# Performance work log

Measured on AMD Instinct MI355X. Metric: run time of the kernel, lower is better.

Reference implementation:

```python
import jax, jax.numpy as jnp
import numpy as np

NUM_EXPERTS = 8
HIDDEN = 1024
INTERMEDIATE = 2816
TOTAL_TOKENS = 4096  # 512 tokens per expert


def setup_inputs() -> dict:
    key = jax.random.key(0)
    k_x, k1, k2, k3 = jax.random.split(key, 4)
    hiddens = jax.random.normal(k_x, (TOTAL_TOKENS, HIDDEN), dtype=jnp.float32)
    # tokens assumed pre-sorted by expert; equal-sized groups here
    batch_sizes = jnp.full((NUM_EXPERTS,), TOTAL_TOKENS // NUM_EXPERTS, dtype=jnp.int64)
    w1_weight = jax.random.normal(k1, (NUM_EXPERTS, HIDDEN, INTERMEDIATE), dtype=jnp.float32)
    w2_weight = jax.random.normal(k2, (NUM_EXPERTS, INTERMEDIATE, HIDDEN), dtype=jnp.float32)
    w3_weight = jax.random.normal(k3, (NUM_EXPERTS, HIDDEN, INTERMEDIATE), dtype=jnp.float32)
    return {
        "hiddens": hiddens,
        "w1_weight": w1_weight,
        "w2_weight": w2_weight,
        "w3_weight": w3_weight,
        "batch_sizes": batch_sizes,
    }


def _grouped_moe(hiddens, w1, w2, w3, batch_sizes):
    """Grouped SwiGLU FFN: tokens are contiguous per expert (sizes = batch_sizes).

    Jit-safe formulation: map each token to its expert id, then run one masked
    dense GEMM trio per expert (small fixed expert count). Zero rows contribute
    exactly zero (silu(0)*0 == 0), so no final masking of the output is needed.
    """
    num_experts = w1.shape[0]
    total_tokens = hiddens.shape[0]
    bounds = jnp.cumsum(batch_sizes)  # [E] exclusive-right boundaries
    expert_ids = jnp.searchsorted(bounds, jnp.arange(total_tokens), side="right")  # [T]
    out = jnp.zeros((total_tokens, w2.shape[-1]), dtype=hiddens.dtype)
    for e in range(num_experts):
        mask = (expert_ids == e)[:, None]  # [T, 1]
        xe = jnp.where(mask, hiddens, 0)   # zero out other experts' tokens
        up = jax.nn.silu(xe @ w1[e]) * (xe @ w3[e])  # [T, F] SwiGLU
        out = out + up @ w2[e]             # [T, H]
    return out


def reference(hiddens, w1_weight, w2_weight, w3_weight, batch_sizes):
    return _grouped_moe(hiddens, w1_weight, w2_weight, w3_weight, batch_sizes)
```

## Files before the change

kernel.cpp:

```cpp
#include <hip/hip_runtime.h>
#include <hip/hip_bf16.h>

#define NE 8
#define HD 1024
#define ID 2816
#define TT 4096
#define BM 128
#define BK 32
#define BN1 64
#define BN2 64
#define MAXMT (TT / BM + NE)
#define NKS1 (HD / BK)
#define NKS2 (ID / BK)
#define ATILE 8192
#define GS 1040
#define BT (4 * GS)

typedef __attribute__((ext_vector_type(4))) float f32x4;
typedef __attribute__((ext_vector_type(8))) short s16x8;

__device__ __forceinline__ unsigned int f2bfpk(float lo, float hi) {
  float2 t; t.x = lo; t.y = hi;
  union { __hip_bfloat162 h2; unsigned int u; } cv;
  cv.h2 = __float22bfloat162_rn(t);
  return cv.u;
}

__device__ __forceinline__ void glds16(const void* g, void* l) {
  __builtin_amdgcn_global_load_lds(
      (const __attribute__((address_space(1))) void*)g,
      (__attribute__((address_space(3))) void*)l, 16, 0, 0);
}

__device__ __forceinline__ bool map_tile(const void* bsp, int mt, int& e,
                                         int& mstart, int& rowend) {
  const int* w = (const int*)bsp;
  bool is64 = (w[1] == 0) && (w[3] == 0) && (w[5] == 0) && (w[7] == 0) &&
              ((w[0] | w[2] | w[4] | w[6]) != 0);
  long long start = 0;
  int rem = mt;
  for (int i = 0; i < NE; ++i) {
    long long b = is64 ? ((const long long*)bsp)[i] : (long long)w[i];
    if (b < 0) b = 0;
    int tiles = (int)((b + BM - 1) / BM);
    if (rem < tiles) {
      long long m0 = start + (long long)rem * BM;
      long long me = start + b;
      if (m0 >= TT) return false;
      if (me > TT) me = TT;
      e = i; mstart = (int)m0; rowend = (int)me;
      return true;
    }
    rem -= tiles;
    start += b;
  }
  return false;
}

__global__ __launch_bounds__(256) void cvt_xt(const float* __restrict__ x,
                                              const void* __restrict__ bsp,
                                              unsigned short* __restrict__ xt) {
  int mt = blockIdx.x >> 5;
  int ks = blockIdx.x & 31;
  int e, mstart, rowend;
  if (!map_tile(bsp, mt, e, mstart, rowend)) return;
  int t = threadIdx.x;
  int lane = t & 63;
  int r = lane & 15, q = lane >> 4;
  unsigned short* ob = xt + ((size_t)mt * NKS1 + ks) * (ATILE / 2);
#pragma unroll
  for (int h = 0; h < 2; ++h) {
    int f = h * 4 + (t >> 6);
    int row = mstart + f * 16 + r;
    s16x8 o = (s16x8)0;
    if (row < rowend) {
      const float* src = x + (size_t)row * HD + ks * 32 + q * 8;
      f32x4 v0 = *(const f32x4*)src;
      f32x4 v1 = *(const f32x4*)(src + 4);
      unsigned int d0 = f2bfpk(v0[0], v0[1]), d1 = f2bfpk(v0[2], v0[3]);
      unsigned int d2 = f2bfpk(v1[0], v1[1]), d3 = f2bfpk(v1[2], v1[3]);
      o[0] = (short)d0; o[1] = (short)(d0 >> 16);
      o[2] = (short)d1; o[3] = (short)(d1 >> 16);
      o[4] = (short)d2; o[5] = (short)(d2 >> 16);
      o[6] = (short)d3; o[7] = (short)(d3 >> 16);
    }
    *(s16x8*)(ob + h * 2048 + t * 8) = o;
  }
}

__global__ __launch_bounds__(256, 3) void moe_gemm1(
    const unsigned short* __restrict__ xt, const float* __restrict__ w1,
    const float* __restrict__ w3, const void* __restrict__ bsp,
    __hip_bfloat16* __restrict__ up) {
  __shared__ __align__(16) char As[2][ATILE];
  __shared__ __align__(16) char B1s[2][BT];
  __shared__ __align__(16) char B3s[2][BT];

  const int NWG = (ID / BN1) * MAXMT;
  int bid = blockIdx.x;
  int logical = (bid & 7) * (NWG >> 3) + (bid >> 3);
  int mt = logical % MAXMT;
  int nt = logical / MAXMT;
  int e, mstart, rowend;
  if (!map_tile(bsp, mt, e, mstart, rowend)) return;
  const int n0 = nt * BN1;
  const int tid = threadIdx.x;
  const int lane = tid & 63;
  const int wv = tid >> 6;
  const int wr = wv >> 1, wc = wv & 1;
  const int q = lane >> 4, r16 = lane & 15;

  const int c4 = tid & 15, kb = tid >> 4;
  const int wbase = (c4 >> 2) * GS + (kb >> 2) * 256 + (c4 & 3) * 64 + (kb & 3) * 4;
  const char* agp = (const char*)xt + (size_t)mt * NKS1 * ATILE + tid * 16;
  const float* w1c = w1 + (size_t)e * HD * ID + (size_t)(2 * kb) * ID + n0 + c4 * 4;
  const float* w3c = w3 + (size_t)e * HD * ID + (size_t)(2 * kb) * ID + n0 + c4 * 4;

  f32x4 acc1[4][2], acc3[4][2];
#pragma unroll
  for (int i = 0; i < 4; ++i)
#pragma unroll
    for (int j = 0; j < 2; ++j) { acc1[i][j] = (f32x4)0.f; acc3[i][j] = (f32x4)0.f; }

  f32x4 Wa[4], Wb[4];

  auto gldsA = [&](int k, int buf) {
    const char* s = agp + (size_t)k * ATILE;
    char* d = &As[buf][0] + tid * 16;
    glds16(s, d);
    glds16(s + 4096, d + 4096);
  };
  auto loadB = [&](f32x4* W) {
    W[0] = *(const f32x4*)w1c;
    W[1] = *(const f32x4*)(w1c + ID);
    W[2] = *(const f32x4*)w3c;
    W[3] = *(const f32x4*)(w3c + ID);
    w1c += (size_t)BK * ID; w3c += (size_t)BK * ID;
  };
  auto storeB = [&](int buf, const f32x4* W) {
#pragma unroll
    for (int ci = 0; ci < 4; ++ci) {
      *(unsigned int*)(B1s[buf] + wbase + ci * 16) = f2bfpk(W[0][ci], W[1][ci]);
      *(unsigned int*)(B3s[buf] + wbase + ci * 16) = f2bfpk(W[2][ci], W[3][ci]);
    }
  };
  auto compute = [&](int ab, int bb) {
    s16x8 a[4], b1[2], b3[2];
#pragma unroll
    for (int i = 0; i < 4; ++i)
      a[i] = *(const s16x8*)(As[ab] + (wr * 4 + i) * 1024 + lane * 16);
#pragma unroll
    for (int j = 0; j < 2; ++j) {
      b1[j] = *(const s16x8*)(B1s[bb] + (wc * 2 + j) * GS + lane * 16);
      b3[j] = *(const s16x8*)(B3s[bb] + (wc * 2 + j) * GS + lane * 16);
    }
#pragma unroll
    for (int i = 0; i < 4; ++i)
#pragma unroll
      for (int j = 0; j < 2; ++j) {
        acc1[i][j] = __builtin_amdgcn_mfma_f32_16x16x32_bf16(a[i], b1[j], acc1[i][j], 0, 0, 0);
        acc3[i][j] = __builtin_amdgcn_mfma_f32_16x16x32_bf16(a[i], b3[j], acc3[i][j], 0, 0, 0);
      }
  };

#define G1PHASE(P, KC)                                                    \
  {                                                                       \
    const bool doG = (kt + (KC) + 1 < NKS1);                              \
    const bool doL = (kt + (KC) + 2 < NKS1);                              \
    if (doG) {                                                            \
      gldsA(kt + (KC) + 1, (P) ^ 1);                                      \
      __builtin_amdgcn_sched_barrier(0);                                  \
    }                                                                     \
    if (doL) {                                                            \
      loadB((P) ? Wb : Wa);                                               \
      __builtin_amdgcn_sched_barrier(0);                                  \
    }                                                                     \
    compute((P), (P));                                                    \
    if (doG) {                                                            \
      storeB((P) ^ 1, (P) ? Wa : Wb);                                     \
      if (doL)                                                            \
        asm volatile("s_waitcnt vmcnt(4) lgkmcnt(0)" ::: "memory");       \
      else                                                                \
        asm volatile("s_waitcnt vmcnt(0) lgkmcnt(0)" ::: "memory");       \
      __builtin_amdgcn_s_barrier();                                       \
    }                                                                     \
  }

  gldsA(0, 0);
  __builtin_amdgcn_sched_barrier(0);
  loadB(Wa);
  __builtin_amdgcn_sched_barrier(0);
  loadB(Wb);
  storeB(0, Wa);
  asm volatile("s_waitcnt vmcnt(4) lgkmcnt(0)" ::: "memory");
  __builtin_amdgcn_s_barrier();

  for (int kt = 0; kt < NKS1; kt += 2) {
    G1PHASE(0, 0)
    G1PHASE(1, 1)
  }
#undef G1PHASE

#pragma unroll
  for (int i = 0; i < 4; ++i)
#pragma unroll
    for (int r = 0; r < 4; ++r) {
      int gm = mstart + wr * 64 + i * 16 + q * 4 + r;
      if (gm < rowend) {
#pragma unroll
        for (int j = 0; j < 2; ++j) {
          float v1 = acc1[i][j][r], v3 = acc3[i][j][r];
          float s = v1 / (1.f + __expf(-v1));
          up[(size_t)gm * ID + n0 + wc * 32 + j * 16 + r16] = __float2bfloat16(s * v3);
        }
      }
    }
}

__global__ __launch_bounds__(256, 4) void moe_gemm2(
    const __hip_bfloat16* __restrict__ up, const float* __restrict__ w2,
    const void* __restrict__ bsp, float* __restrict__ out) {
  __shared__ __align__(16) char As[2][ATILE];
  __shared__ __align__(16) char Bs[2][BT];

  const int NWG = (HD / BN2) * MAXMT;
  int bid = blockIdx.x;
  int logical = (bid & 7) * (NWG >> 3) + (bid >> 3);
  int mt = logical % MAXMT;
  int nt = logical / MAXMT;
  int e, mstart, rowend;
  if (!map_tile(bsp, mt, e, mstart, rowend)) return;
  const int n0 = nt * BN2;
  const int tid = threadIdx.x;
  const int lane = tid & 63;
  const int wv = tid >> 6;
  const int wr = wv >> 1, wc = wv & 1;
  const int q = lane >> 4, r16 = lane & 15;

  const int c4 = tid & 15, kb = tid >> 4;
  const int wbase = (c4 >> 2) * GS + (kb >> 2) * 256 + (c4 & 3) * 64 + (kb & 3) * 4;
  const float* w2c = w2 + (size_t)e * ID * HD + (size_t)(2 * kb) * HD + n0 + c4 * 4;

  int row0 = mstart + (tid >> 6) * 16 + (tid & 15);
  int row1 = row0 + 64;
  row0 = row0 < TT ? row0 : TT - 1;
  row1 = row1 < TT ? row1 : TT - 1;
  const char* uc0 = (const char*)up + ((size_t)row0 * ID + q * 8) * 2;
  const char* uc1 = (const char*)up + ((size_t)row1 * ID + q * 8) * 2;

  f32x4 acc[4][2];
#pragma unroll
  for (int i = 0; i < 4; ++i)
#pragma unroll
    for (int j = 0; j < 2; ++j) acc[i][j] = (f32x4)0.f;

  f32x4 Wa[2], Wb[2];

  auto gldsA = [&](int buf) {
    char* d = &As[buf][0] + tid * 16;
    glds16(uc0, d);
    glds16(uc1, d + 4096);
    uc0 += BK * 2; uc1 += BK * 2;
  };
  auto loadB = [&](f32x4* W) {
    W[0] = *(const f32x4*)w2c;
    W[1] = *(const f32x4*)(w2c + HD);
    w2c += (size_t)BK * HD;
  };
  auto storeB = [&](int buf, const f32x4* W) {
#pragma unroll
    for (int ci = 0; ci < 4; ++ci)
      *(unsigned int*)(Bs[buf] + wbase + ci * 16) = f2bfpk(W[0][ci], W[1][ci]);
  };
  auto compute = [&](int ab, int bb) {
    s16x8 a[4], b[2];
#pragma unroll
    for (int i = 0; i < 4; ++i)
      a[i] = *(const s16x8*)(As[ab] + (wr * 4 + i) * 1024 + lane * 16);
#pragma unroll
    for (int j = 0; j < 2; ++j)
      b[j] = *(const s16x8*)(Bs[bb] + (wc * 2 + j) * GS + lane * 16);
#pragma unroll
    for (int i = 0; i < 4; ++i)
#pragma unroll
      for (int j = 0; j < 2; ++j)
        acc[i][j] = __builtin_amdgcn_mfma_f32_16x16x32_bf16(a[i], b[j], acc[i][j], 0, 0, 0);
  };

#define G2PHASE(P, KC)                                                    \
  {                                                                       \
    const bool doG = (kt + (KC) + 1 < NKS2);                              \
    const bool doL = (kt + (KC) + 2 < NKS2);                              \
    if (doG) {                                                            \
      gldsA((P) ^ 1);                                                     \
      __builtin_amdgcn_sched_barrier(0);                                  \
    }                                                                     \
    if (doL) {                                                            \
      loadB((P) ? Wb : Wa);                                               \
      __builtin_amdgcn_sched_barrier(0);                                  \
    }                                                                     \
    compute((P), (P));                                                    \
    if (doG) {                                                            \
      storeB((P) ^ 1, (P) ? Wa : Wb);                                     \
      if (doL)                                                            \
        asm volatile("s_waitcnt vmcnt(2) lgkmcnt(0)" ::: "memory");       \
      else                                                                \
        asm volatile("s_waitcnt vmcnt(0) lgkmcnt(0)" ::: "memory");       \
      __builtin_amdgcn_s_barrier();                                       \
    }                                                                     \
  }

  gldsA(0);
  __builtin_amdgcn_sched_barrier(0);
  loadB(Wa);
  __builtin_amdgcn_sched_barrier(0);
  loadB(Wb);
  storeB(0, Wa);
  asm volatile("s_waitcnt vmcnt(2) lgkmcnt(0)" ::: "memory");
  __builtin_amdgcn_s_barrier();

  for (int kt = 0; kt < NKS2; kt += 2) {
    G2PHASE(0, 0)
    G2PHASE(1, 1)
  }
#undef G2PHASE

#pragma unroll
  for (int i = 0; i < 4; ++i)
#pragma unroll
    for (int r = 0; r < 4; ++r) {
      int gm = mstart + wr * 64 + i * 16 + q * 4 + r;
      if (gm < rowend) {
#pragma unroll
        for (int j = 0; j < 2; ++j)
          out[(size_t)gm * HD + n0 + wc * 32 + j * 16 + r16] = acc[i][j][r];
      }
    }
}

extern "C" void kernel_launch(void* const* d_in, const int* in_sizes, int n_in,
                              void* d_out, int out_size, void* d_ws, size_t ws_size,
                              hipStream_t stream) {
  const float* x = (const float*)d_in[0];
  const float* w1 = (const float*)d_in[1];
  const float* w2 = (const float*)d_in[2];
  const float* w3 = (const float*)d_in[3];
  const void* bs = d_in[4];
  float* out = (float*)d_out;
  unsigned short* xt = (unsigned short*)d_ws;
  __hip_bfloat16* up =
      (__hip_bfloat16*)((char*)d_ws + (size_t)MAXMT * NKS1 * ATILE);

  hipMemsetAsync(d_out, 0, (size_t)out_size * sizeof(float), stream);

  cvt_xt<<<dim3(MAXMT * NKS1), dim3(256), 0, stream>>>(x, bs, xt);
  moe_gemm1<<<dim3((ID / BN1) * MAXMT), dim3(256), 0, stream>>>(xt, w1, w3, bs, up);
  moe_gemm2<<<dim3((HD / BN2) * MAXMT), dim3(256), 0, stream>>>(up, w2, bs, out);
}
```

Measured before the change: 199.7 us.

## Widen N tiles to 128 with 512-thread blocks and simplify B prefetch pipeline

Both grouped GEMMs move from 64-wide to 128-wide N tiles on 512-thread workgroups. Each of the 8 waves keeps the same 64x32 output sub-tile, and the global-to-LDS load work is spread across twice as many threads. The two-deep register prefetch of B is cut to a single prefetch with a full vmcnt(0) wait, which saves registers but exposes more load latency per step. s_setprio is wrapped around the MFMA block to favour compute waves, and the larger tile roughly halves how often A is re-read across N tiles, at the cost of fewer workgroups.

```diff
diff --git a/kernel.cpp b/kernel.cpp
--- a/kernel.cpp
+++ b/kernel.cpp
@@ -7,14 +7,14 @@
 #define TT 4096
 #define BM 128
 #define BK 32
-#define BN1 64
-#define BN2 64
+#define BN1 128
+#define BN2 128
 #define MAXMT (TT / BM + NE)
 #define NKS1 (HD / BK)
 #define NKS2 (ID / BK)
 #define ATILE 8192
 #define GS 1040
-#define BT (4 * GS)
+#define BT (8 * GS)
 
 typedef __attribute__((ext_vector_type(4))) float f32x4;
 typedef __attribute__((ext_vector_type(8))) short s16x8;
@@ -88,7 +88,7 @@
   }
 }
 
-__global__ __launch_bounds__(256, 3) void moe_gemm1(
+__global__ __launch_bounds__(512, 4) void moe_gemm1(
     const unsigned short* __restrict__ xt, const float* __restrict__ w1,
     const float* __restrict__ w3, const void* __restrict__ bsp,
     __hip_bfloat16* __restrict__ up) {
@@ -107,11 +107,12 @@
   const int tid = threadIdx.x;
   const int lane = tid & 63;
   const int wv = tid >> 6;
-  const int wr = wv >> 1, wc = wv & 1;
+  const int wr = wv >> 2, wc = wv & 3;
   const int q = lane >> 4, r16 = lane & 15;
 
-  const int c4 = tid & 15, kb = tid >> 4;
-  const int wbase = (c4 >> 2) * GS + (kb >> 2) * 256 + (c4 & 3) * 64 + (kb & 3) * 4;
+  const int c4 = tid & 31, kb = tid >> 5;
+  const int wbase = (c4 >> 2) * GS + (kb >> 2) * 256 + (kb & 3) * 4;
+  const int wcol = (c4 & 3) * 4;
   const char* agp = (const char*)xt + (size_t)mt * NKS1 * ATILE + tid * 16;
   const float* w1c = w1 + (size_t)e * HD * ID + (size_t)(2 * kb) * ID + n0 + c4 * 4;
   const float* w3c = w3 + (size_t)e * HD * ID + (size_t)(2 * kb) * ID + n0 + c4 * 4;
@@ -122,26 +123,23 @@
 #pragma unroll
     for (int j = 0; j < 2; ++j) { acc1[i][j] = (f32x4)0.f; acc3[i][j] = (f32x4)0.f; }
 
-  f32x4 Wa[4], Wb[4];
+  f32x4 W1[2], W3[2];
 
   auto gldsA = [&](int k, int buf) {
-    const char* s = agp + (size_t)k * ATILE;
-    char* d = &As[buf][0] + tid * 16;
-    glds16(s, d);
-    glds16(s + 4096, d + 4096);
-  };
-  auto loadB = [&](f32x4* W) {
-    W[0] = *(const f32x4*)w1c;
-    W[1] = *(const f32x4*)(w1c + ID);
-    W[2] = *(const f32x4*)w3c;
-    W[3] = *(const f32x4*)(w3c + ID);
+    glds16(agp + (size_t)k * ATILE, &As[buf][0] + tid * 16);
+  };
+  auto loadB = [&]() {
+    W1[0] = *(const f32x4*)w1c;
+    W1[1] = *(const f32x4*)(w1c + ID);
+    W3[0] = *(const f32x4*)w3c;
+    W3[1] = *(const f32x4*)(w3c + ID);
     w1c += (size_t)BK * ID; w3c += (size_t)BK * ID;
   };
-  auto storeB = [&](int buf, const f32x4* W) {
+  auto storeB = [&](int buf) {
 #pragma unroll
     for (int ci = 0; ci < 4; ++ci) {
-      *(unsigned int*)(B1s[buf] + wbase + ci * 16) = f2bfpk(W[0][ci], W[1][ci]);
-      *(unsigned int*)(B3s[buf] + wbase + ci * 16) = f2bfpk(W[2][ci], W[3][ci]);
+      *(unsigned int*)(B1s[buf] + wbase + (wcol + ci) * 16) = f2bfpk(W1[0][ci], W1[1][ci]);
+      *(unsigned int*)(B3s[buf] + wbase + (wcol + ci) * 16) = f2bfpk(W3[0][ci], W3[1][ci]);
     }
   };
   auto compute = [&](int ab, int bb) {
@@ -154,6 +152,7 @@
       b1[j] = *(const s16x8*)(B1s[bb] + (wc * 2 + j) * GS + lane * 16);
       b3[j] = *(const s16x8*)(B3s[bb] + (wc * 2 + j) * GS + lane * 16);
     }
+    __builtin_amdgcn_s_setprio(1);
 #pragma unroll
     for (int i = 0; i < 4; ++i)
 #pragma unroll
@@ -161,38 +160,31 @@
         acc1[i][j] = __builtin_amdgcn_mfma_f32_16x16x32_bf16(a[i], b1[j], acc1[i][j], 0, 0, 0);
         acc3[i][j] = __builtin_amdgcn_mfma_f32_16x16x32_bf16(a[i], b3[j], acc3[i][j], 0, 0, 0);
       }
+    __builtin_amdgcn_s_setprio(0);
   };
 
 #define G1PHASE(P, KC)                                                    \
   {                                                                       \
-    const bool doG = (kt + (KC) + 1 < NKS1);                              \
-    const bool doL = (kt + (KC) + 2 < NKS1);                              \
-    if (doG) {                                                            \
+    const bool nx = (kt + (KC) + 1 < NKS1);                               \
+    if (nx) {                                                             \
+      loadB();                                                            \
+      __builtin_amdgcn_sched_barrier(0);                                  \
       gldsA(kt + (KC) + 1, (P) ^ 1);                                      \
       __builtin_amdgcn_sched_barrier(0);                                  \
     }                                                                     \
-    if (doL) {                                                            \
-      loadB((P) ? Wb : Wa);                                               \
-      __builtin_amdgcn_sched_barrier(0);                                  \
-    }                                                                     \
     compute((P), (P));                                                    \
-    if (doG) {                                                            \
-      storeB((P) ^ 1, (P) ? Wa : Wb);                                     \
-      if (doL)                                                            \
-        asm volatile("s_waitcnt vmcnt(4) lgkmcnt(0)" ::: "memory");       \
-      else                                                                \
-        asm volatile("s_waitcnt vmcnt(0) lgkmcnt(0)" ::: "memory");       \
+    if (nx) {                                                             \
+      storeB((P) ^ 1);                                                    \
+      asm volatile("s_waitcnt vmcnt(0) lgkmcnt(0)" ::: "memory");         \
       __builtin_amdgcn_s_barrier();                                       \
     }                                                                     \
   }
 
+  loadB();
+  __builtin_amdgcn_sched_barrier(0);
   gldsA(0, 0);
-  __builtin_amdgcn_sched_barrier(0);
-  loadB(Wa);
-  __builtin_amdgcn_sched_barrier(0);
-  loadB(Wb);
-  storeB(0, Wa);
-  asm volatile("s_waitcnt vmcnt(4) lgkmcnt(0)" ::: "memory");
+  storeB(0);
+  asm volatile("s_waitcnt vmcnt(0) lgkmcnt(0)" ::: "memory");
   __builtin_amdgcn_s_barrier();
 
   for (int kt = 0; kt < NKS1; kt += 2) {
@@ -217,7 +209,7 @@
     }
 }
 
-__global__ __launch_bounds__(256, 4) void moe_gemm2(
+__global__ __launch_bounds__(512, 4) void moe_gemm2(
     const __hip_bfloat16* __restrict__ up, const float* __restrict__ w2,
     const void* __restrict__ bsp, float* __restrict__ out) {
   __shared__ __align__(16) char As[2][ATILE];
@@ -234,19 +226,17 @@
   const int tid = threadIdx.x;
   const int lane = tid & 63;
   const int wv = tid >> 6;
-  const int wr = wv >> 1, wc = wv & 1;
+  const int wr = wv >> 2, wc = wv & 3;
   const int q = lane >> 4, r16 = lane & 15;
 
-  const int c4 = tid & 15, kb = tid >> 4;
-  const int wbase = (c4 >> 2) * GS + (kb >> 2) * 256 + (c4 & 3) * 64 + (kb & 3) * 4;
+  const int c4 = tid & 31, kb = tid >> 5;
+  const int wbase = (c4 >> 2) * GS + (kb >> 2) * 256 + (kb & 3) * 4;
+  const int wcol = (c4 & 3) * 4;
   const float* w2c = w2 + (size_t)e * ID * HD + (size_t)(2 * kb) * HD + n0 + c4 * 4;
 
   int row0 = mstart + (tid >> 6) * 16 + (tid & 15);
-  int row1 = row0 + 64;
   row0 = row0 < TT ? row0 : TT - 1;
-  row1 = row1 < TT ? row1 : TT - 1;
-  const char* uc0 = (const char*)up + ((size_t)row0 * ID + q * 8) * 2;
-  const char* uc1 = (const char*)up + ((size_t)row1 * ID + q * 8) * 2;
+  const char* uc0 = (const char*)up + ((size_t)row0 * ID + ((tid >> 4) & 3) * 8) * 2;
 
   f32x4 acc[4][2];
 #pragma unroll
@@ -254,23 +244,21 @@
 #pragma unroll
     for (int j = 0; j < 2; ++j) acc[i][j] = (f32x4)0.f;
 
-  f32x4 Wa[2], Wb[2];
+  f32x4 W[2];
 
   auto gldsA = [&](int buf) {
-    char* d = &As[buf][0] + tid * 16;
-    glds16(uc0, d);
-    glds16(uc1, d + 4096);
-    uc0 += BK * 2; uc1 += BK * 2;
-  };
-  auto loadB = [&](f32x4* W) {
+    glds16(uc0, &As[buf][0] + tid * 16);
+    uc0 += BK * 2;
+  };
+  auto loadB = [&]() {
     W[0] = *(const f32x4*)w2c;
     W[1] = *(const f32x4*)(w2c + HD);
     w2c += (size_t)BK * HD;
   };
-  auto storeB = [&](int buf, const f32x4* W) {
+  auto storeB = [&](int buf) {
 #pragma unroll
     for (int ci = 0; ci < 4; ++ci)
-      *(unsigned int*)(Bs[buf] + wbase + ci * 16) = f2bfpk(W[0][ci], W[1][ci]);
+      *(unsigned int*)(Bs[buf] + wbase + (wcol + ci) * 16) = f2bfpk(W[0][ci], W[1][ci]);
   };
   auto compute = [&](int ab, int bb) {
     s16x8 a[4], b[2];
@@ -280,43 +268,37 @@
 #pragma unroll
     for (int j = 0; j < 2; ++j)
       b[j] = *(const s16x8*)(Bs[bb] + (wc * 2 + j) * GS + lane * 16);
+    __builtin_amdgcn_s_setprio(1);
 #pragma unroll
     for (int i = 0; i < 4; ++i)
 #pragma unroll
       for (int j = 0; j < 2; ++j)
         acc[i][j] = __builtin_amdgcn_mfma_f32_16x16x32_bf16(a[i], b[j], acc[i][j], 0, 0, 0);
+    __builtin_amdgcn_s_setprio(0);
   };
 
 #define G2PHASE(P, KC)                                                    \
   {                                                                       \
-    const bool doG = (kt + (KC) + 1 < NKS2);                              \
-    const bool doL = (kt + (KC) + 2 < NKS2);                              \
-    if (doG) {                                                            \
+    const bool nx = (kt + (KC) + 1 < NKS2);                               \
+    if (nx) {                                                             \
+      loadB();                                                            \
+      __builtin_amdgcn_sched_barrier(0);                                  \
       gldsA((P) ^ 1);                                                     \
       __builtin_amdgcn_sched_barrier(0);                                  \
     }                                                                     \
-    if (doL) {                                                            \
-      loadB((P) ? Wb : Wa);                                               \
-      __builtin_amdgcn_sched_barrier(0);                                  \
-    }                                                                     \
     compute((P), (P));                                                    \
-    if (doG) {                                                            \
-      storeB((P) ^ 1, (P) ? Wa : Wb);                                     \
-      if (doL)                                                            \
-        asm volatile("s_waitcnt vmcnt(2) lgkmcnt(0)" ::: "memory");       \
-      else                                                                \
-        asm volatile("s_waitcnt vmcnt(0) lgkmcnt(0)" ::: "memory");       \
+    if (nx) {                                                             \
+      storeB((P) ^ 1);                                                    \
+      asm volatile("s_waitcnt vmcnt(0) lgkmcnt(0)" ::: "memory");         \
       __builtin_amdgcn_s_barrier();                                       \
     }                                                                     \
   }
 
+  loadB();
+  __builtin_amdgcn_sched_barrier(0);
   gldsA(0);
-  __builtin_amdgcn_sched_barrier(0);
-  loadB(Wa);
-  __builtin_amdgcn_sched_barrier(0);
-  loadB(Wb);
-  storeB(0, Wa);
-  asm volatile("s_waitcnt vmcnt(2) lgkmcnt(0)" ::: "memory");
+  storeB(0);
+  asm volatile("s_waitcnt vmcnt(0) lgkmcnt(0)" ::: "memory");
   __builtin_amdgcn_s_barrier();
 
   for (int kt = 0; kt < NKS2; kt += 2) {
@@ -354,6 +336,6 @@
   hipMemsetAsync(d_out, 0, (size_t)out_size * sizeof(float), stream);
 
   cvt_xt<<<dim3(MAXMT * NKS1), dim3(256), 0, stream>>>(x, bs, xt);
-  moe_gemm1<<<dim3((ID / BN1) * MAXMT), dim3(256), 0, stream>>>(xt, w1, w3, bs, up);
-  moe_gemm2<<<dim3((HD / BN2) * MAXMT), dim3(256), 0, stream>>>(up, w2, bs, out);
-}
+  moe_gemm1<<<dim3((ID / BN1) * MAXMT), dim3(512), 0, stream>>>(xt, w1, w3, bs, up);
+  moe_gemm2<<<dim3((HD / BN2) * MAXMT), dim3(512), 0, stream>>>(up, w2, bs, out);
+}
```

New measurement: 250.0 us. 25.2% more time.

## Double M tile to 256 rows with 512-thread blocks and MFMA priority

Applied to the files above, without the earlier changes.

Raises the M tile from 128 to 256 rows and runs both GEMMs with 512-thread blocks (8 waves). Each block now reuses every converted fp32 weight tile across twice as many tokens. This halves the per-token weight global reads and the fp32-to-bf16 conversion work, which dominate since weights are fp32. In gemm1 the W1 and W3 loads are split between the two halves of the block; in gemm2 only half the threads load W2. MFMA sections are wrapped in s_setprio, and the waitcnt counts are adjusted. Risks are fewer blocks per expert, more LDS per block, and tile waste when expert groups do not fill 256 rows.

```diff
diff --git a/kernel.cpp b/kernel.cpp
--- a/kernel.cpp
+++ b/kernel.cpp
@@ -5,7 +5,7 @@
 #define HD 1024
 #define ID 2816
 #define TT 4096
-#define BM 128
+#define BM 256
 #define BK 32
 #define BN1 64
 #define BN2 64
@@ -13,6 +13,7 @@
 #define NKS1 (HD / BK)
 #define NKS2 (ID / BK)
 #define ATILE 8192
+#define TILE2 (2 * ATILE)
 #define GS 1040
 #define BT (4 * GS)
 
@@ -67,11 +68,12 @@
   int t = threadIdx.x;
   int lane = t & 63;
   int r = lane & 15, q = lane >> 4;
-  unsigned short* ob = xt + ((size_t)mt * NKS1 + ks) * (ATILE / 2);
-#pragma unroll
-  for (int h = 0; h < 2; ++h) {
-    int f = h * 4 + (t >> 6);
-    int row = mstart + f * 16 + r;
+  unsigned short* ob = xt + ((size_t)mt * NKS1 + ks) * (TILE2 / 2);
+#pragma unroll
+  for (int hh = 0; hh < 4; ++hh) {
+    int half = hh >> 1, fq = hh & 1;
+    int f = fq * 4 + (t >> 6);
+    int row = mstart + half * 128 + f * 16 + r;
     s16x8 o = (s16x8)0;
     if (row < rowend) {
       const float* src = x + (size_t)row * HD + ks * 32 + q * 8;
@@ -84,15 +86,15 @@
       o[4] = (short)d2; o[5] = (short)(d2 >> 16);
       o[6] = (short)d3; o[7] = (short)(d3 >> 16);
     }
-    *(s16x8*)(ob + h * 2048 + t * 8) = o;
-  }
-}
-
-__global__ __launch_bounds__(256, 3) void moe_gemm1(
+    *(s16x8*)(ob + half * 4096 + fq * 2048 + t * 8) = o;
+  }
+}
+
+__global__ __launch_bounds__(512, 2) void moe_gemm1(
     const unsigned short* __restrict__ xt, const float* __restrict__ w1,
     const float* __restrict__ w3, const void* __restrict__ bsp,
     __hip_bfloat16* __restrict__ up) {
-  __shared__ __align__(16) char As[2][ATILE];
+  __shared__ __align__(16) char As[2][TILE2];
   __shared__ __align__(16) char B1s[2][BT];
   __shared__ __align__(16) char B3s[2][BT];
 
@@ -110,11 +112,15 @@
   const int wr = wv >> 1, wc = wv & 1;
   const int q = lane >> 4, r16 = lane & 15;
 
-  const int c4 = tid & 15, kb = tid >> 4;
-  const int wbase = (c4 >> 2) * GS + (kb >> 2) * 256 + (c4 & 3) * 64 + (kb & 3) * 4;
-  const char* agp = (const char*)xt + (size_t)mt * NKS1 * ATILE + tid * 16;
-  const float* w1c = w1 + (size_t)e * HD * ID + (size_t)(2 * kb) * ID + n0 + c4 * 4;
-  const float* w3c = w3 + (size_t)e * HD * ID + (size_t)(2 * kb) * ID + n0 + c4 * 4;
+  const int t8 = tid & 255;
+  const int c4 = t8 & 15, kp = t8 >> 4;
+  const int wbase = (c4 >> 2) * GS + (kp >> 2) * 256 + (kp & 3) * 4;
+  const int wcol = (c4 & 3) * 4;
+  const char* agp = (const char*)xt + (size_t)mt * NKS1 * TILE2 + tid * 16;
+  const float* wsrc = ((tid & 256) ? w3 : w1) + (size_t)e * HD * ID +
+                      (size_t)(2 * kp) * ID + n0 + c4 * 4;
+  char* bdst0 = (tid & 256) ? B3s[0] : B1s[0];
+  char* bdst1 = (tid & 256) ? B3s[1] : B1s[1];
 
   f32x4 acc1[4][2], acc3[4][2];
 #pragma unroll
@@ -122,38 +128,37 @@
 #pragma unroll
     for (int j = 0; j < 2; ++j) { acc1[i][j] = (f32x4)0.f; acc3[i][j] = (f32x4)0.f; }
 
-  f32x4 Wa[4], Wb[4];
+  f32x4 Wa[2], Wb[2];
 
   auto gldsA = [&](int k, int buf) {
-    const char* s = agp + (size_t)k * ATILE;
+    const char* s = agp + (size_t)k * TILE2;
     char* d = &As[buf][0] + tid * 16;
     glds16(s, d);
-    glds16(s + 4096, d + 4096);
+    glds16(s + ATILE, d + ATILE);
   };
   auto loadB = [&](f32x4* W) {
-    W[0] = *(const f32x4*)w1c;
-    W[1] = *(const f32x4*)(w1c + ID);
-    W[2] = *(const f32x4*)w3c;
-    W[3] = *(const f32x4*)(w3c + ID);
-    w1c += (size_t)BK * ID; w3c += (size_t)BK * ID;
+    W[0] = *(const f32x4*)wsrc;
+    W[1] = *(const f32x4*)(wsrc + ID);
+    wsrc += (size_t)BK * ID;
   };
   auto storeB = [&](int buf, const f32x4* W) {
-#pragma unroll
-    for (int ci = 0; ci < 4; ++ci) {
-      *(unsigned int*)(B1s[buf] + wbase + ci * 16) = f2bfpk(W[0][ci], W[1][ci]);
-      *(unsigned int*)(B3s[buf] + wbase + ci * 16) = f2bfpk(W[2][ci], W[3][ci]);
-    }
+    char* b = buf ? bdst1 : bdst0;
+#pragma unroll
+    for (int ci = 0; ci < 4; ++ci)
+      *(unsigned int*)(b + wbase + (wcol + ci) * 16) = f2bfpk(W[0][ci], W[1][ci]);
   };
   auto compute = [&](int ab, int bb) {
     s16x8 a[4], b1[2], b3[2];
 #pragma unroll
     for (int i = 0; i < 4; ++i)
-      a[i] = *(const s16x8*)(As[ab] + (wr * 4 + i) * 1024 + lane * 16);
+      a[i] = *(const s16x8*)(As[ab] + (wr >> 1) * ATILE +
+                             ((wr & 1) * 4 + i) * 1024 + lane * 16);
 #pragma unroll
     for (int j = 0; j < 2; ++j) {
       b1[j] = *(const s16x8*)(B1s[bb] + (wc * 2 + j) * GS + lane * 16);
       b3[j] = *(const s16x8*)(B3s[bb] + (wc * 2 + j) * GS + lane * 16);
     }
+    __builtin_amdgcn_s_setprio(1);
 #pragma unroll
     for (int i = 0; i < 4; ++i)
 #pragma unroll
@@ -161,6 +166,7 @@
         acc1[i][j] = __builtin_amdgcn_mfma_f32_16x16x32_bf16(a[i], b1[j], acc1[i][j], 0, 0, 0);
         acc3[i][j] = __builtin_amdgcn_mfma_f32_16x16x32_bf16(a[i], b3[j], acc3[i][j], 0, 0, 0);
       }
+    __builtin_amdgcn_s_setprio(0);
   };
 
 #define G1PHASE(P, KC)                                                    \
@@ -179,7 +185,7 @@
     if (doG) {                                                            \
       storeB((P) ^ 1, (P) ? Wa : Wb);                                     \
       if (doL)                                                            \
-        asm volatile("s_waitcnt vmcnt(4) lgkmcnt(0)" ::: "memory");       \
+        asm volatile("s_waitcnt vmcnt(2) lgkmcnt(0)" ::: "memory");       \
       else                                                                \
         asm volatile("s_waitcnt vmcnt(0) lgkmcnt(0)" ::: "memory");       \
       __builtin_amdgcn_s_barrier();                                       \
@@ -192,7 +198,7 @@
   __builtin_amdgcn_sched_barrier(0);
   loadB(Wb);
   storeB(0, Wa);
-  asm volatile("s_waitcnt vmcnt(4) lgkmcnt(0)" ::: "memory");
+  asm volatile("s_waitcnt vmcnt(2) lgkmcnt(0)" ::: "memory");
   __builtin_amdgcn_s_barrier();
 
   for (int kt = 0; kt < NKS1; kt += 2) {
@@ -217,10 +223,10 @@
     }
 }
 
-__global__ __launch_bounds__(256, 4) void moe_gemm2(
+__global__ __launch_bounds__(512, 2) void moe_gemm2(
     const __hip_bfloat16* __restrict__ up, const float* __restrict__ w2,
     const void* __restrict__ bsp, float* __restrict__ out) {
-  __shared__ __align__(16) char As[2][ATILE];
+  __shared__ __align__(16) char As[2][TILE2];
   __shared__ __align__(16) char Bs[2][BT];
 
   const int NWG = (HD / BN2) * MAXMT;
@@ -237,16 +243,18 @@
   const int wr = wv >> 1, wc = wv & 1;
   const int q = lane >> 4, r16 = lane & 15;
 
-  const int c4 = tid & 15, kb = tid >> 4;
-  const int wbase = (c4 >> 2) * GS + (kb >> 2) * 256 + (c4 & 3) * 64 + (kb & 3) * 4;
-  const float* w2c = w2 + (size_t)e * ID * HD + (size_t)(2 * kb) * HD + n0 + c4 * 4;
-
-  int row0 = mstart + (tid >> 6) * 16 + (tid & 15);
-  int row1 = row0 + 64;
-  row0 = row0 < TT ? row0 : TT - 1;
-  row1 = row1 < TT ? row1 : TT - 1;
-  const char* uc0 = (const char*)up + ((size_t)row0 * ID + q * 8) * 2;
-  const char* uc1 = (const char*)up + ((size_t)row1 * ID + q * 8) * 2;
+  const int c4 = tid & 15, kp = (tid >> 4) & 15;
+  const int wbase = (c4 >> 2) * GS + (kp >> 2) * 256 + (kp & 3) * 4;
+  const int wcol = (c4 & 3) * 4;
+  const float* wsrc = w2 + (size_t)e * ID * HD + (size_t)(2 * kp) * HD + n0 + c4 * 4;
+
+  const char* uc[2];
+#pragma unroll
+  for (int h = 0; h < 2; ++h) {
+    int row = mstart + h * 128 + ((tid >> 6) * 16) + (tid & 15);
+    row = row < TT ? row : TT - 1;
+    uc[h] = (const char*)up + ((size_t)row * ID + ((tid >> 4) & 3) * 8) * 2;
+  }
 
   f32x4 acc[4][2];
 #pragma unroll
@@ -258,33 +266,40 @@
 
   auto gldsA = [&](int buf) {
     char* d = &As[buf][0] + tid * 16;
-    glds16(uc0, d);
-    glds16(uc1, d + 4096);
-    uc0 += BK * 2; uc1 += BK * 2;
+    glds16(uc[0], d);
+    glds16(uc[1], d + ATILE);
+    uc[0] += BK * 2; uc[1] += BK * 2;
   };
   auto loadB = [&](f32x4* W) {
-    W[0] = *(const f32x4*)w2c;
-    W[1] = *(const f32x4*)(w2c + HD);
-    w2c += (size_t)BK * HD;
+    if (tid < 256) {
+      W[0] = *(const f32x4*)wsrc;
+      W[1] = *(const f32x4*)(wsrc + HD);
+    }
+    wsrc += (size_t)BK * HD;
   };
   auto storeB = [&](int buf, const f32x4* W) {
-#pragma unroll
-    for (int ci = 0; ci < 4; ++ci)
-      *(unsigned int*)(Bs[buf] + wbase + ci * 16) = f2bfpk(W[0][ci], W[1][ci]);
+    if (tid < 256) {
+#pragma unroll
+      for (int ci = 0; ci < 4; ++ci)
+        *(unsigned int*)(Bs[buf] + wbase + (wcol + ci) * 16) = f2bfpk(W[0][ci], W[1][ci]);
+    }
   };
   auto compute = [&](int ab, int bb) {
     s16x8 a[4], b[2];
 #pragma unroll
     for (int i = 0; i < 4; ++i)
-      a[i] = *(const s16x8*)(As[ab] + (wr * 4 + i) * 1024 + lane * 16);
+      a[i] = *(const s16x8*)(As[ab] + (wr >> 1) * ATILE +
+                             ((wr & 1) * 4 + i) * 1024 + lane * 16);
 #pragma unroll
     for (int j = 0; j < 2; ++j)
       b[j] = *(const s16x8*)(Bs[bb] + (wc * 2 + j) * GS + lane * 16);
+    __builtin_amdgcn_s_setprio(1);
 #pragma unroll
     for (int i = 0; i < 4; ++i)
 #pragma unroll
       for (int j = 0; j < 2; ++j)
         acc[i][j] = __builtin_amdgcn_mfma_f32_16x16x32_bf16(a[i], b[j], acc[i][j], 0, 0, 0);
+    __builtin_amdgcn_s_setprio(0);
   };
 
 #define G2PHASE(P, KC)                                                    \
@@ -349,11 +364,11 @@
   float* out = (float*)d_out;
   unsigned short* xt = (unsigned short*)d_ws;
   __hip_bfloat16* up =
-      (__hip_bfloat16*)((char*)d_ws + (size_t)MAXMT * NKS1 * ATILE);
+      (__hip_bfloat16*)((char*)d_ws + (size_t)MAXMT * NKS1 * TILE2);
 
   hipMemsetAsync(d_out, 0, (size_t)out_size * sizeof(float), stream);
 
   cvt_xt<<<dim3(MAXMT * NKS1), dim3(256), 0, stream>>>(x, bs, xt);
-  moe_gemm1<<<dim3((ID / BN1) * MAXMT), dim3(256), 0, stream>>>(xt, w1, w3, bs, up);
-  moe_gemm2<<<dim3((HD / BN2) * MAXMT), dim3(256), 0, stream>>>(up, w2, bs, out);
-}
+  moe_gemm1<<<dim3((ID / BN1) * MAXMT), dim3(512), 0, stream>>>(xt, w1, w3, bs, up);
+  moe_gemm2<<<dim3((HD / BN2) * MAXMT), dim3(512), 0, stream>>>(up, w2, bs, out);
+}
```

New measurement: 249.0 us. 24.7% more time.
